# Optimization experiments

Hardware: AMD Instinct MI355X
Metric: run time of the kernel (lower is better)

## Reference

```python
import jax, jax.numpy as jnp
import numpy as np

BATCH, SEQ, D_MODEL, K_SIZE = 2, 4096, 2048, 3


def setup_inputs() -> dict:
    key = jax.random.key(0)
    k1, k2, k3, k4 = jax.random.split(key, 4)
    s = 1.0 / np.sqrt(D_MODEL)
    x = jax.random.normal(k1, (BATCH, SEQ, D_MODEL), dtype=jnp.float32)
    w1 = jax.random.normal(k2, (3 * D_MODEL, D_MODEL), dtype=jnp.float32) * s
    w2 = jax.random.normal(k3, (D_MODEL, D_MODEL), dtype=jnp.float32) * s
    conv_w = jax.random.normal(k4, (D_MODEL, 1, K_SIZE), dtype=jnp.float32) * 0.5
    return {"x": x, "w1": w1, "w2": w2, "conv_w": conv_w}


def _causal_depthwise_conv(u, conv_w):
    # u: [B, D, S]; conv_w: [D, 1, K] (torch Conv1d weight layout, groups=D)
    k = conv_w.shape[-1]
    return jax.lax.conv_general_dilated(
        u, conv_w,
        window_strides=(1,),
        padding=[(k - 1, 0)],  # left pad = causal; matches pad=k-1 then [..., :seq_len]
        feature_group_count=u.shape[1],
        dimension_numbers=("NCH", "OIH", "NCH"),
    )


def reference(x, w1, w2, conv_w):
    # x: [B, S, D]
    BCx = jnp.einsum("bsd,ed->bse", x, w1)           # [B, S, 3D]
    Bg, Cg, Xg = jnp.split(BCx, 3, axis=-1)           # each [B, S, D]
    u = (Bg * Xg).transpose(0, 2, 1)                  # [B, D, S]
    conv_out = _causal_depthwise_conv(u, conv_w)      # [B, D, S]
    gated = Cg * conv_out.transpose(0, 2, 1)          # [B, S, D]
    return jnp.einsum("bsd,ed->bse", gated, w2)       # [B, S, D]
```

## Files before the change

### kernel.cpp

```cpp
#include <hip/hip_runtime.h>
#include <stdint.h>

#define BATCH 2
#define SEQ   4096
#define DM    2048
#define MT    (BATCH*SEQ)
#define N1    (3*DM)
#define STRIP 8

typedef __attribute__((ext_vector_type(8)))  __bf16 bf16x8;
typedef __attribute__((ext_vector_type(16))) float  f32x16;
typedef __attribute__((ext_vector_type(8)))  unsigned short ushort8v;
typedef __attribute__((ext_vector_type(4)))  unsigned short ushort4v;

__device__ inline unsigned short f2bf(float f) {
    uint32_t u = __float_as_uint(f);
    u += 0x7FFFu + ((u >> 16) & 1u);
    return (unsigned short)(u >> 16);
}
__device__ inline float bf2f(unsigned short h) {
    return __uint_as_float(((uint32_t)h) << 16);
}

__global__ void cvt_all_bf16(const float* __restrict__ s0, int n0,
                             const float* __restrict__ s1, int n1,
                             const float* __restrict__ s2,
                             unsigned short* __restrict__ dst) {
    const int i = (blockIdx.x * blockDim.x + threadIdx.x) << 3;
    const float* src;
    int off;
    if (i < n0)            { src = s0; off = i; }
    else if (i < n0 + n1)  { src = s1; off = i - n0; }
    else                   { src = s2; off = i - n0 - n1; }
    const float4 a = *(const float4*)(src + off);
    const float4 b = *(const float4*)(src + off + 4);
    ushort8v o;
    o[0] = f2bf(a.x); o[1] = f2bf(a.y); o[2] = f2bf(a.z); o[3] = f2bf(a.w);
    o[4] = f2bf(b.x); o[5] = f2bf(b.y); o[6] = f2bf(b.z); o[7] = f2bf(b.w);
    *(ushort8v*)(dst + i) = o;
}

__device__ inline void async_copy16(const void* g, void* l) {
    __builtin_amdgcn_global_load_lds(
        (const __attribute__((address_space(1))) void*)g,
        (__attribute__((address_space(3))) void*)l,
        16, 0, 0);
}

#define MFMA32_(d, a, b) d = __builtin_amdgcn_mfma_f32_32x32x16_bf16(a, b, d, 0, 0, 0)

#define M8_32(FR) do { \
  MFMA32_(acc[0][0], FR[0], FR[4]); \
  MFMA32_(acc[0][1], FR[0], FR[5]); \
  MFMA32_(acc[1][0], FR[1], FR[4]); \
  MFMA32_(acc[1][1], FR[1], FR[5]); \
  MFMA32_(acc[2][0], FR[2], FR[4]); \
  MFMA32_(acc[2][1], FR[2], FR[5]); \
  MFMA32_(acc[3][0], FR[3], FR[4]); \
  MFMA32_(acc[3][1], FR[3], FR[5]); \
} while (0)

template <bool OUT_BF16>
__global__ __launch_bounds__(512, 1)
void gemm256(const unsigned short* __restrict__ A,
             const unsigned short* __restrict__ B,
             void* __restrict__ Cout, int M, int N, int K) {
    __shared__ __attribute__((aligned(16))) char lds[131072];
    const int tid  = threadIdx.x;
    const int wave = tid >> 6;
    const int lane = tid & 63;
    const int wr = wave >> 2, wc = wave & 3;
    const int NT = K >> 6;

    const int nx = gridDim.x;
    int flat = blockIdx.y * nx + blockIdx.x;
    const int cpx = (nx * gridDim.y) >> 3;
    flat = (flat & 7) * cpx + (flat >> 3);
    const int blockN = (flat % nx) << 8;
    const int blockM = (flat / nx) << 8;

    const int swze = ((((lane & 7) << 4) ^ ((lane >> 3) << 4)) >> 1);
    const int sr   = (wave << 3) + (lane >> 3);
    const unsigned short* Ab = A + (size_t)blockM * K;
    const unsigned short* Bb = B + (size_t)blockN * K;
    const size_t a00 = (size_t)(sr      ) * K + swze;
    const size_t a01 = (size_t)(sr +  64) * K + swze;
    const size_t a10 = (size_t)(sr + 128) * K + swze;
    const size_t a11 = (size_t)(sr + 192) * K + swze;
    const int bsr = ((wave >> 2) << 6) + ((wave & 3) << 3) + (lane >> 3);
    const size_t b00 = (size_t)(bsr      ) * K + swze;
    const size_t b01 = (size_t)(bsr + 128) * K + swze;
    const size_t b10 = (size_t)(bsr +  32) * K + swze;
    const size_t b11 = (size_t)(bsr + 160) * K + swze;
    const int ldsw = wave << 10;

#define STG_A(BUF, U, K0) do { \
    async_copy16(Ab + a##U##0 + (K0), lds + (BUF) + (U)*16384 + ldsw); \
    async_copy16(Ab + a##U##1 + (K0), lds + (BUF) + (U)*16384 + 8192 + ldsw); } while (0)
#define STG_B(BUF, NH, K0) do { \
    async_copy16(Bb + b##NH##0 + (K0), lds + (BUF) + 32768 + (NH)*16384 + ldsw); \
    async_copy16(Bb + b##NH##1 + (K0), lds + (BUF) + 32768 + (NH)*16384 + 8192 + ldsw); } while (0)

    const int l31  = lane & 31;
    const int kh   = (lane >> 5) << 4;
    const int fswz = (lane & 7) << 4;
    const int cS0 = (  0 + kh) ^ fswz;
    const int cS1 = ( 32 + kh) ^ fswz;
    const int cS2 = ( 64 + kh) ^ fswz;
    const int cS3 = ( 96 + kh) ^ fswz;
    const int aB32 = wr * 16384 + l31 * 128;
    const int bB32 = 32768 + (wc * 32 + l31) * 128;

#define LDA32_(BUF, MI, C) (*(const bf16x8*)(lds + (BUF) + aB32 + (MI)*4096 + (C)))
#define LDB32_(BUF, NI, C) (*(const bf16x8*)(lds + (BUF) + bB32 + (NI)*16384 + (C)))
#define RD_S(DST, BUF, C) do { \
    DST[0] = LDA32_(BUF, 0, C); DST[1] = LDA32_(BUF, 1, C); \
    DST[2] = LDA32_(BUF, 2, C); DST[3] = LDA32_(BUF, 3, C); \
    DST[4] = LDB32_(BUF, 0, C); DST[5] = LDB32_(BUF, 1, C); } while (0)

    f32x16 acc[4][2] = {};
    bf16x8 fP[6], fQ[6];

    STG_B(0, 0, 0); STG_B(0, 1, 0); STG_A(0, 0, 0); STG_A(0, 1, 0);
    if (NT > 1) {
        STG_B(65536, 0, 64); STG_B(65536, 1, 64);
        STG_A(65536, 0, 64); STG_A(65536, 1, 64);
    }
    asm volatile("s_waitcnt vmcnt(0)" ::: "memory");
    __builtin_amdgcn_s_barrier();
    RD_S(fP, 0, cS0);

#define SP1 __builtin_amdgcn_s_setprio(1)
#define SP0 __builtin_amdgcn_s_setprio(0)

#define ITER(CUR, NXT, T) do { \
     \
    __builtin_amdgcn_s_barrier(); \
    if ((T) >= 1 && (T) + 1 < NT) { \
        STG_A(NXT, 0, ((T)+1)*64); STG_A(NXT, 1, ((T)+1)*64); \
        STG_B(NXT, 0, ((T)+1)*64); STG_B(NXT, 1, ((T)+1)*64); \
    } \
    RD_S(fQ, CUR, cS1); \
    SP1; M8_32(fP); SP0; \
     \
    RD_S(fP, CUR, cS2); \
    SP1; M8_32(fQ); SP0; \
     \
    RD_S(fQ, CUR, cS3); \
    SP1; M8_32(fP); SP0; \
     \
    if ((T) + 1 < NT) { \
        asm volatile("s_waitcnt vmcnt(0)" ::: "memory"); \
        __builtin_amdgcn_s_barrier(); \
        RD_S(fP, NXT, cS0); \
    } \
    SP1; M8_32(fQ); SP0; \
} while (0)

    for (int t = 0; t < NT; t += 2) {
        ITER(0, 65536, t);
        ITER(65536, 0, t + 1);
    }

    const int orow = blockM + wr * 128 + ((lane >> 5) << 2);
    const int ocol = blockN + wc * 64 + l31;
    #pragma unroll
    for (int mi = 0; mi < 4; ++mi) {
        #pragma unroll
        for (int ni = 0; ni < 2; ++ni) {
            #pragma unroll
            for (int r = 0; r < 16; ++r) {
                const int row = orow + mi * 32 + (r & 3) + ((r >> 2) << 3);
                const int col = ocol + ni * 32;
                if constexpr (OUT_BF16)
                    ((unsigned short*)Cout)[(size_t)row * N + col] = f2bf(acc[mi][ni][r]);
                else
                    ((float*)Cout)[(size_t)row * N + col] = acc[mi][ni][r];
            }
        }
    }
#undef ITER
#undef RD_S
#undef LDA32_
#undef LDB32_
#undef STG_A
#undef STG_B
}

__global__ void conv_gate_kernel(const unsigned short* __restrict__ BCx,
                                 const float* __restrict__ cw,
                                 unsigned short* __restrict__ gated) {
    const int tid = threadIdx.x;
    const int d0  = tid * 8;
    const int nstrips = SEQ / STRIP;
    const int b   = blockIdx.x / nstrips;
    const int s0  = (blockIdx.x % nstrips) * STRIP;

    float w0[8], w1c[8], w2c[8];
    #pragma unroll
    for (int c = 0; c < 8; ++c) {
        w0[c]  = cw[(d0 + c) * 3 + 0];
        w1c[c] = cw[(d0 + c) * 3 + 1];
        w2c[c] = cw[(d0 + c) * 3 + 2];
    }

    float um1[8], um2[8];
    if (s0 > 0) {
        const unsigned short* r2 = BCx + (size_t)(b * SEQ + s0 - 2) * N1;
        const unsigned short* r1 = BCx + (size_t)(b * SEQ + s0 - 1) * N1;
        ushort8v bg2 = *(const ushort8v*)(r2 + d0);
        ushort8v xg2 = *(const ushort8v*)(r2 + 2 * DM + d0);
        ushort8v bg1 = *(const ushort8v*)(r1 + d0);
        ushort8v xg1 = *(const ushort8v*)(r1 + 2 * DM + d0);
        #pragma unroll
        for (int c = 0; c < 8; ++c) {
            um2[c] = bf2f(bg2[c]) * bf2f(xg2[c]);
            um1[c] = bf2f(bg1[c]) * bf2f(xg1[c]);
        }
    } else {
        #pragma unroll
        for (int c = 0; c < 8; ++c) { um2[c] = 0.f; um1[c] = 0.f; }
    }

    for (int s = s0; s < s0 + STRIP; ++s) {
        const size_t m = (size_t)b * SEQ + s;
        const unsigned short* rp = BCx + m * N1;
        ushort8v bg = *(const ushort8v*)(rp + d0);
        ushort8v cg = *(const ushort8v*)(rp + DM + d0);
        ushort8v xg = *(const ushort8v*)(rp + 2 * DM + d0);
        ushort8v og;
        #pragma unroll
        for (int c = 0; c < 8; ++c) {
            const float u    = bf2f(bg[c]) * bf2f(xg[c]);
            const float conv = w0[c] * um2[c] + w1c[c] * um1[c] + w2c[c] * u;
            const float g    = bf2f(cg[c]) * conv;
            um2[c] = um1[c];
            um1[c] = u;
            og[c]  = f2bf(g);
        }
        *(ushort8v*)(gated + m * DM + d0) = og;
    }
}

extern "C" void kernel_launch(void* const* d_in, const int* in_sizes, int n_in,
                              void* d_out, int out_size, void* d_ws, size_t ws_size,
                              hipStream_t stream) {
    const float* x   = (const float*)d_in[0];
    const float* w1  = (const float*)d_in[1];
    const float* w2  = (const float*)d_in[2];
    const float* cw  = (const float*)d_in[3];
    float* out = (float*)d_out;

    char* ws = (char*)d_ws;
    unsigned short* x_bf   = (unsigned short*)ws;
    unsigned short* w1_bf  = x_bf  + (size_t)MT * DM;
    unsigned short* w2_bf  = w1_bf + (size_t)N1 * DM;
    unsigned short* bcx_bf = w2_bf + (size_t)DM * DM;
    unsigned short* g_bf   = bcx_bf + (size_t)MT * N1;

    cvt_all_bf16<<<16384, 256, 0, stream>>>(x,  MT * DM,
                                            w1, N1 * DM,
                                            w2, x_bf);

    gemm256<true><<<dim3(N1 / 256, MT / 256), 512, 0, stream>>>(
        x_bf, w1_bf, bcx_bf, MT, N1, DM);

    conv_gate_kernel<<<BATCH * (SEQ / STRIP), 256, 0, stream>>>(bcx_bf, cw, g_bf);

    gemm256<false><<<dim3(DM / 256, MT / 256), 512, 0, stream>>>(
        g_bf, w2_bf, out, MT, DM, DM);
}
```

Measured before the change: 329.7 us.

## Stage GEMM tiles in fragment-major LDS layout for conflict-free contiguous reads

Changes how global tiles are laid out in LDS. Each wave now copies 32 rows by 8-column chunks arranged so that every MFMA fragment read is one contiguous 1KB block indexed by lane, replacing the XOR-swizzled row-major layout. This simplifies LDS read address math and is meant to keep ds_read free of bank conflicts. The trade-off is that global loads become less coalesced, since each lane now reads 16 bytes from a different row instead of 8 lanes covering one 128-byte row segment.

```diff
diff --git a/kernel.cpp b/kernel.cpp
--- a/kernel.cpp
+++ b/kernel.cpp
@@ -79,44 +79,33 @@
     const int blockN = (flat % nx) << 8;
     const int blockM = (flat / nx) << 8;
 
-    const int swze = ((((lane & 7) << 4) ^ ((lane >> 3) << 4)) >> 1);
-    const int sr   = (wave << 3) + (lane >> 3);
+    const int rbase = ((wave >> 2) << 5) + (lane & 31);
+    const int colk  = ((wave & 3) << 4) + ((lane >> 5) << 3);
     const unsigned short* Ab = A + (size_t)blockM * K;
     const unsigned short* Bb = B + (size_t)blockN * K;
-    const size_t a00 = (size_t)(sr      ) * K + swze;
-    const size_t a01 = (size_t)(sr +  64) * K + swze;
-    const size_t a10 = (size_t)(sr + 128) * K + swze;
-    const size_t a11 = (size_t)(sr + 192) * K + swze;
-    const int bsr = ((wave >> 2) << 6) + ((wave & 3) << 3) + (lane >> 3);
-    const size_t b00 = (size_t)(bsr      ) * K + swze;
-    const size_t b01 = (size_t)(bsr + 128) * K + swze;
-    const size_t b10 = (size_t)(bsr +  32) * K + swze;
-    const size_t b11 = (size_t)(bsr + 160) * K + swze;
+    const size_t o00 = (size_t)(rbase      ) * K + colk;
+    const size_t o01 = (size_t)(rbase +  64) * K + colk;
+    const size_t o10 = (size_t)(rbase + 128) * K + colk;
+    const size_t o11 = (size_t)(rbase + 192) * K + colk;
     const int ldsw = wave << 10;
 
 #define STG_A(BUF, U, K0) do { \
-    async_copy16(Ab + a##U##0 + (K0), lds + (BUF) + (U)*16384 + ldsw); \
-    async_copy16(Ab + a##U##1 + (K0), lds + (BUF) + (U)*16384 + 8192 + ldsw); } while (0)
-#define STG_B(BUF, NH, K0) do { \
-    async_copy16(Bb + b##NH##0 + (K0), lds + (BUF) + 32768 + (NH)*16384 + ldsw); \
-    async_copy16(Bb + b##NH##1 + (K0), lds + (BUF) + 32768 + (NH)*16384 + 8192 + ldsw); } while (0)
-
-    const int l31  = lane & 31;
-    const int kh   = (lane >> 5) << 4;
-    const int fswz = (lane & 7) << 4;
-    const int cS0 = (  0 + kh) ^ fswz;
-    const int cS1 = ( 32 + kh) ^ fswz;
-    const int cS2 = ( 64 + kh) ^ fswz;
-    const int cS3 = ( 96 + kh) ^ fswz;
-    const int aB32 = wr * 16384 + l31 * 128;
-    const int bB32 = 32768 + (wc * 32 + l31) * 128;
-
-#define LDA32_(BUF, MI, C) (*(const bf16x8*)(lds + (BUF) + aB32 + (MI)*4096 + (C)))
-#define LDB32_(BUF, NI, C) (*(const bf16x8*)(lds + (BUF) + bB32 + (NI)*16384 + (C)))
-#define RD_S(DST, BUF, C) do { \
-    DST[0] = LDA32_(BUF, 0, C); DST[1] = LDA32_(BUF, 1, C); \
-    DST[2] = LDA32_(BUF, 2, C); DST[3] = LDA32_(BUF, 3, C); \
-    DST[4] = LDB32_(BUF, 0, C); DST[5] = LDB32_(BUF, 1, C); } while (0)
+    async_copy16(Ab + o##U##0 + (K0), lds + (BUF) + (U)*16384 + ldsw); \
+    async_copy16(Ab + o##U##1 + (K0), lds + (BUF) + (U)*16384 + 8192 + ldsw); } while (0)
+#define STG_B(BUF, U, K0) do { \
+    async_copy16(Bb + o##U##0 + (K0), lds + (BUF) + 32768 + (U)*16384 + ldsw); \
+    async_copy16(Bb + o##U##1 + (K0), lds + (BUF) + 32768 + (U)*16384 + 8192 + ldsw); } while (0)
+
+    const int rdl  = lane << 4;
+    const int aFT  = (wr << 2) * 4096;
+    const int bFT  = 32768 + (wc << 1) * 4096;
+
+#define LDA32_(BUF, MI, S) (*(const bf16x8*)(lds + (BUF) + aFT + (MI)*4096 + (S)*1024 + rdl))
+#define LDB32_(BUF, NI, S) (*(const bf16x8*)(lds + (BUF) + bFT + (NI)*4096 + (S)*1024 + rdl))
+#define RD_S(DST, BUF, S) do { \
+    DST[0] = LDA32_(BUF, 0, S); DST[1] = LDA32_(BUF, 1, S); \
+    DST[2] = LDA32_(BUF, 2, S); DST[3] = LDA32_(BUF, 3, S); \
+    DST[4] = LDB32_(BUF, 0, S); DST[5] = LDB32_(BUF, 1, S); } while (0)
 
     f32x16 acc[4][2] = {};
     bf16x8 fP[6], fQ[6];
@@ -128,7 +117,7 @@
     }
     asm volatile("s_waitcnt vmcnt(0)" ::: "memory");
     __builtin_amdgcn_s_barrier();
-    RD_S(fP, 0, cS0);
+    RD_S(fP, 0, 0);
 
 #define SP1 __builtin_amdgcn_s_setprio(1)
 #define SP0 __builtin_amdgcn_s_setprio(0)
@@ -140,19 +129,19 @@
         STG_A(NXT, 0, ((T)+1)*64); STG_A(NXT, 1, ((T)+1)*64); \
         STG_B(NXT, 0, ((T)+1)*64); STG_B(NXT, 1, ((T)+1)*64); \
     } \
-    RD_S(fQ, CUR, cS1); \
+    RD_S(fQ, CUR, 1); \
     SP1; M8_32(fP); SP0; \
      \
-    RD_S(fP, CUR, cS2); \
+    RD_S(fP, CUR, 2); \
     SP1; M8_32(fQ); SP0; \
      \
-    RD_S(fQ, CUR, cS3); \
+    RD_S(fQ, CUR, 3); \
     SP1; M8_32(fP); SP0; \
      \
     if ((T) + 1 < NT) { \
         asm volatile("s_waitcnt vmcnt(0)" ::: "memory"); \
         __builtin_amdgcn_s_barrier(); \
-        RD_S(fP, NXT, cS0); \
+        RD_S(fP, NXT, 0); \
     } \
     SP1; M8_32(fQ); SP0; \
 } while (0)
@@ -162,6 +151,7 @@
         ITER(65536, 0, t + 1);
     }
 
+    const int l31  = lane & 31;
     const int orow = blockM + wr * 128 + ((lane >> 5) << 2);
     const int ocol = blockN + wc * 64 + l31;
     #pragma unroll
```

Measured after the change: 393.5 us. 19.3% more time.
